# Kernel optimization log

Hardware: AMD Instinct MI355X
Metric: run time of the kernel (lower is better)

The kernel has to match this reference:

```python
import jax, jax.numpy as jnp
import numpy as np

EPS = 1e-7  # K.epsilon()


def setup_inputs() -> dict:
    key = jax.random.key(0)
    k1, k2, k3, k4 = jax.random.split(key, 4)
    B, T, S = 512, 32, 2048  # batch, time_steps, seq_len
    inputs = jax.random.normal(k1, (B, T, S), dtype=jnp.float32)
    # Keras mask (float 0/1), same shape as inputs
    mask = (jax.random.uniform(k2, (B, T, S)) < 0.8).astype(jnp.float32)
    # 'uniform' keras initializer: U(-0.05, 0.05)
    W = jax.random.uniform(k3, (S, T, T), minval=-0.05, maxval=0.05, dtype=jnp.float32)
    b = jax.random.uniform(k4, (S, T), minval=-0.05, maxval=0.05, dtype=jnp.float32)
    return {"inputs": inputs, "mask": mask, "W": W, "b": b}


def reference(inputs, mask, W, b):
    # (B,T,S) -> (B,S,T), apply mask
    x = jnp.transpose(inputs, (0, 2, 1)) * jnp.transpose(mask, (0, 2, 1))
    # per-position matmul, batched over B and S (replaces the tf.scan over batch)
    z = jnp.einsum('bst,stu->bsu', x, W) + b  # (B,S,T)
    e = jnp.exp(jnp.tanh(z))
    att = e / (jnp.sum(e, axis=2, keepdims=True) + EPS)  # softmax-like over T
    return jnp.sum(att * x, axis=1)  # (B,T)
```

## Files before the change

### kernel.cpp

```cpp
#include <hip/hip_runtime.h>

#define EPS_K 1e-7f

typedef __attribute__((ext_vector_type(8)))  short          frag8;
typedef __attribute__((ext_vector_type(16))) float          accf16;
typedef __attribute__((ext_vector_type(4)))  unsigned short us4;

__device__ __forceinline__ unsigned f2bf(float f) {
  union { float f; unsigned u; } v; v.f = f;
  unsigned u = v.u;
  u += 0x7FFFu + ((u >> 16) & 1u);
  return u >> 16;
}
__device__ __forceinline__ float bf2f(unsigned short s) {
  union { unsigned u; float f; } v; v.u = ((unsigned)s) << 16;
  return v.f;
}
__device__ __forceinline__ unsigned pk_bf16(float lo, float hi) {
  return f2bf(lo) | (f2bf(hi) << 16);
}

__global__ __launch_bounds__(256) void wbf_prep(
    const float* __restrict__ Wt, unsigned short* __restrict__ Wbf)
{
  __shared__ unsigned short tile[32 * 33];
  const int s   = blockIdx.x;
  const int tid = threadIdx.x;
  {
    const int t  = tid >> 3;
    const int uc = tid & 7;
    const float4 v = *(const float4*)(Wt + s * 1024 + t * 32 + 4 * uc);
    tile[t * 33 + 4 * uc + 0] = (unsigned short)f2bf(v.x);
    tile[t * 33 + 4 * uc + 1] = (unsigned short)f2bf(v.y);
    tile[t * 33 + 4 * uc + 2] = (unsigned short)f2bf(v.z);
    tile[t * 33 + 4 * uc + 3] = (unsigned short)f2bf(v.w);
  }
  __syncthreads();
  {
    const int u  = tid >> 3;
    const int tc = tid & 7;
    uint2 d;
    d.x = (unsigned)tile[(4 * tc + 0) * 33 + u] | ((unsigned)tile[(4 * tc + 1) * 33 + u] << 16);
    d.y = (unsigned)tile[(4 * tc + 2) * 33 + u] | ((unsigned)tile[(4 * tc + 3) * 33 + u] << 16);
    *(uint2*)(Wbf + s * 1024 + u * 32 + 4 * tc) = d;
  }
}

template <bool WBF, bool USE_WS>
__global__ __launch_bounds__(256, 5) void attn_fused(
    const float* __restrict__ inp,
    const float* __restrict__ msk,
    const float* __restrict__ Wt,
    const unsigned short* __restrict__ Wbf,
    const float* __restrict__ bias,
    float* __restrict__ part,
    float* __restrict__ out)
{
  __shared__ unsigned short x_us[32 * 512];

  const int tid = threadIdx.x;
  const int st  = blockIdx.x >> 4;
  const int bg  = blockIdx.x & 15;
  const int s0  = st * 16;

  #pragma unroll
  for (int iter = 0; iter < 2; ++iter) {
    const int idx = iter * 256 + tid;
    const int sc  = idx & 3;
    const int tb  = (idx >> 2) & 3;
    const int b   = idx >> 4;
    const float* ip = inp + ((size_t)(bg * 32 + b) * 32 + 8 * tb) * 2048 + s0 + 4 * sc;
    const float* mp = msk + ((size_t)(bg * 32 + b) * 32 + 8 * tb) * 2048 + s0 + 4 * sc;
    unsigned c32[4][4];
    #pragma unroll
    for (int j2 = 0; j2 < 4; ++j2) {
      const float4 vi0 = *(const float4*)(ip + (2 * j2)     * 2048);
      const float4 vm0 = *(const float4*)(mp + (2 * j2)     * 2048);
      const float4 vi1 = *(const float4*)(ip + (2 * j2 + 1) * 2048);
      const float4 vm1 = *(const float4*)(mp + (2 * j2 + 1) * 2048);
      c32[0][j2] = pk_bf16(vi0.x * vm0.x, vi1.x * vm1.x);
      c32[1][j2] = pk_bf16(vi0.y * vm0.y, vi1.y * vm1.y);
      c32[2][j2] = pk_bf16(vi0.z * vm0.z, vi1.z * vm1.z);
      c32[3][j2] = pk_bf16(vi0.w * vm0.w, vi1.w * vm1.w);
    }
    #pragma unroll
    for (int w = 0; w < 4; ++w) {
      const int L = tb * 16 + 4 * sc + w;
      unsigned* dst = (unsigned*)(x_us + b * 512 + ((L ^ (b & 7)) * 8));
      *(uint4*)dst = make_uint4(c32[w][0], c32[w][1], c32[w][2], c32[w][3]);
    }
  }
  __syncthreads();

  const int lane = tid & 63;
  const int wv   = tid >> 6;
  const int n    = lane & 31;
  const int h    = lane >> 5;
  const int nx   = n & 7;

  float O[16];
  #pragma unroll
  for (int r = 0; r < 16; ++r) O[r] = 0.f;

  #pragma unroll
  for (int si = 0; si < 4; ++si) {
    const int sl = wv * 4 + si;
    const int s  = s0 + sl;

    frag8 a1, a2;
    if (WBF) {
      const unsigned short* wp = Wbf + s * 1024 + n * 32 + 8 * h;
      a1 = *(const frag8*)(wp);
      a2 = *(const frag8*)(wp + 16);
    } else {
      const float* Wp = Wt + s * 1024;
      #pragma unroll
      for (int j = 0; j < 8; ++j) {
        const int t1 = 8 * h + j;
        a1[j] = (short)f2bf(Wp[t1 * 32 + n]);
        a2[j] = (short)f2bf(Wp[(t1 + 16) * 32 + n]);
      }
    }

    const frag8 b1 = *(const frag8*)(x_us + n * 512 + (((h      * 16 + sl) ^ nx) * 8));
    const frag8 b2 = *(const frag8*)(x_us + n * 512 + ((((h + 2) * 16 + sl) ^ nx) * 8));

    accf16 acc;
    #pragma unroll
    for (int g = 0; g < 4; ++g) {
      const float4 bb = *(const float4*)(bias + s * 32 + 8 * g + 4 * h);
      acc[4 * g + 0] = bb.x; acc[4 * g + 1] = bb.y;
      acc[4 * g + 2] = bb.z; acc[4 * g + 3] = bb.w;
    }
    acc = __builtin_amdgcn_mfma_f32_32x32x16_bf16(a1, b1, acc, 0, 0, 0);
    acc = __builtin_amdgcn_mfma_f32_32x32x16_bf16(a2, b2, acc, 0, 0, 0);

    float e[16];
    float ps = 0.f;
    #pragma unroll
    for (int r = 0; r < 16; ++r) {
      const float z  = acc[r];
      const float e2 = __expf(2.f * z);
      const float th = 1.f - 2.f / (e2 + 1.f);
      e[r] = __expf(th);
      ps  += e[r];
    }
    const float tot = ps + __shfl_xor(ps, 32, 64);
    const float inv = 1.f / (tot + EPS_K);

    #pragma unroll
    for (int g = 0; g < 4; ++g) {
      const us4 xv = *(const us4*)(x_us + n * 512 + (((g * 16 + sl) ^ nx) * 8) + 4 * h);
      #pragma unroll
      for (int i = 0; i < 4; ++i)
        O[4 * g + i] += e[4 * g + i] * inv * bf2f(xv[i]);
    }
  }

  __syncthreads();
  float* red = (float*)x_us;
  #pragma unroll
  for (int r = 0; r < 16; ++r) {
    const int u = (r & 3) + 8 * (r >> 2) + 4 * h;
    red[wv * 1024 + n * 32 + (u ^ n)] = O[r];
  }
  __syncthreads();

  const int q0 = tid * 4;
  float4 v;
  float* vp = (float*)&v;
  #pragma unroll
  for (int i = 0; i < 4; ++i) {
    const int q = q0 + i;
    const int b = q >> 5, u = q & 31;
    float sum = 0.f;
    #pragma unroll
    for (int w = 0; w < 4; ++w) sum += red[w * 1024 + b * 32 + (u ^ b)];
    vp[i] = sum;
  }
  if (USE_WS) {
    *(float4*)(part + (size_t)st * 16384 + bg * 1024 + q0) = v;
  } else {
    float* op = out + bg * 1024 + q0;
    #pragma unroll
    for (int i = 0; i < 4; ++i) atomicAdd(op + i, vp[i]);
  }
}

__global__ __launch_bounds__(256) void reduce_part(
    const float* __restrict__ part, float* __restrict__ out)
{
  const int f = blockIdx.x * 256 + threadIdx.x;
  float s = 0.f;
  #pragma unroll 8
  for (int st = 0; st < 128; ++st) s += part[(size_t)st * 16384 + f];
  out[f] = s;
}

extern "C" void kernel_launch(void* const* d_in, const int* in_sizes, int n_in,
                              void* d_out, int out_size, void* d_ws, size_t ws_size,
                              hipStream_t stream) {
  const float* inp  = (const float*)d_in[0];
  const float* msk  = (const float*)d_in[1];
  const float* Wt   = (const float*)d_in[2];
  const float* bias = (const float*)d_in[3];
  float* out = (float*)d_out;

  const size_t part_sz = (size_t)128 * 16384 * sizeof(float);
  const size_t wbf_sz  = (size_t)2048 * 1024 * sizeof(unsigned short);

  if (ws_size >= part_sz + wbf_sz) {
    float* part = (float*)d_ws;
    unsigned short* Wbf = (unsigned short*)((char*)d_ws + part_sz);
    wbf_prep<<<dim3(2048), dim3(256), 0, stream>>>(Wt, Wbf);
    attn_fused<true, true><<<dim3(2048), dim3(256), 0, stream>>>(
        inp, msk, Wt, Wbf, bias, part, out);
    reduce_part<<<dim3(64), dim3(256), 0, stream>>>(part, out);
  } else if (ws_size >= part_sz) {
    float* part = (float*)d_ws;
    attn_fused<false, true><<<dim3(2048), dim3(256), 0, stream>>>(
        inp, msk, Wt, nullptr, bias, part, out);
    reduce_part<<<dim3(64), dim3(256), 0, stream>>>(part, out);
  } else {
    (void)hipMemsetAsync(out, 0, (size_t)out_size * sizeof(float), stream);
    attn_fused<false, false><<<dim3(2048), dim3(256), 0, stream>>>(
        inp, msk, Wt, nullptr, bias, nullptr, out);
  }
}
```

Baseline: 332.2 us.

## Halve per-block sequence tile, double grid, reduce via atomics instead of partials

Each block now handles 8 sequence positions instead of 16, so the grid doubles to 4096 blocks and LDS per block halves, which allows more resident blocks. The partial-sum workspace and the separate reduce kernel are removed. Each block instead atomically adds its results into a zeroed output, and the exp results reuse the accumulator registers. This trades one extra launch and the partial-buffer traffic for 4096×1024 float atomics, which can contend and make the summation order nondeterministic.

Result: faster. 322.2 us (-3.0%).

```diff
diff --git a/kernel.cpp b/kernel.cpp
--- a/kernel.cpp
+++ b/kernel.cpp
@@ -46,29 +46,26 @@
   }
 }
 
-template <bool WBF, bool USE_WS>
+template <bool WBF>
 __global__ __launch_bounds__(256, 5) void attn_fused(
     const float* __restrict__ inp,
     const float* __restrict__ msk,
     const float* __restrict__ Wt,
     const unsigned short* __restrict__ Wbf,
     const float* __restrict__ bias,
-    float* __restrict__ part,
     float* __restrict__ out)
 {
-  __shared__ unsigned short x_us[32 * 512];
+  __shared__ unsigned short x_us[32 * 256];
 
   const int tid = threadIdx.x;
   const int st  = blockIdx.x >> 4;
   const int bg  = blockIdx.x & 15;
-  const int s0  = st * 16;
+  const int s0  = st * 8;
 
-  #pragma unroll
-  for (int iter = 0; iter < 2; ++iter) {
-    const int idx = iter * 256 + tid;
-    const int sc  = idx & 3;
-    const int tb  = (idx >> 2) & 3;
-    const int b   = idx >> 4;
+  {
+    const int sc = tid & 1;
+    const int tb = (tid >> 1) & 3;
+    const int b  = tid >> 3;
     const float* ip = inp + ((size_t)(bg * 32 + b) * 32 + 8 * tb) * 2048 + s0 + 4 * sc;
     const float* mp = msk + ((size_t)(bg * 32 + b) * 32 + 8 * tb) * 2048 + s0 + 4 * sc;
     unsigned c32[4][4];
@@ -85,8 +82,8 @@
     }
     #pragma unroll
     for (int w = 0; w < 4; ++w) {
-      const int L = tb * 16 + 4 * sc + w;
-      unsigned* dst = (unsigned*)(x_us + b * 512 + ((L ^ (b & 7)) * 8));
+      const int L = tb * 8 + 4 * sc + w;
+      unsigned* dst = (unsigned*)(x_us + b * 256 + ((L ^ (b & 7)) * 8));
       *(uint4*)dst = make_uint4(c32[w][0], c32[w][1], c32[w][2], c32[w][3]);
     }
   }
@@ -103,8 +100,8 @@
   for (int r = 0; r < 16; ++r) O[r] = 0.f;
 
   #pragma unroll
-  for (int si = 0; si < 4; ++si) {
-    const int sl = wv * 4 + si;
+  for (int si = 0; si < 2; ++si) {
+    const int sl = wv * 2 + si;
     const int s  = s0 + sl;
 
     frag8 a1, a2;
@@ -122,8 +119,8 @@
       }
     }
 
-    const frag8 b1 = *(const frag8*)(x_us + n * 512 + (((h      * 16 + sl) ^ nx) * 8));
-    const frag8 b2 = *(const frag8*)(x_us + n * 512 + ((((h + 2) * 16 + sl) ^ nx) * 8));
+    const frag8 b1 = *(const frag8*)(x_us + n * 256 + (((h      * 8 + sl) ^ nx) * 8));
+    const frag8 b2 = *(const frag8*)(x_us + n * 256 + ((((h + 2) * 8 + sl) ^ nx) * 8));
 
     accf16 acc;
     #pragma unroll
@@ -135,25 +132,24 @@
     acc = __builtin_amdgcn_mfma_f32_32x32x16_bf16(a1, b1, acc, 0, 0, 0);
     acc = __builtin_amdgcn_mfma_f32_32x32x16_bf16(a2, b2, acc, 0, 0, 0);
 
-    float e[16];
     float ps = 0.f;
     #pragma unroll
     for (int r = 0; r < 16; ++r) {
       const float z  = acc[r];
       const float e2 = __expf(2.f * z);
       const float th = 1.f - 2.f / (e2 + 1.f);
-      e[r] = __expf(th);
-      ps  += e[r];
+      acc[r] = __expf(th);
+      ps    += acc[r];
     }
     const float tot = ps + __shfl_xor(ps, 32, 64);
     const float inv = 1.f / (tot + EPS_K);
 
     #pragma unroll
     for (int g = 0; g < 4; ++g) {
-      const us4 xv = *(const us4*)(x_us + n * 512 + (((g * 16 + sl) ^ nx) * 8) + 4 * h);
+      const us4 xv = *(const us4*)(x_us + n * 256 + (((g * 8 + sl) ^ nx) * 8) + 4 * h);
       #pragma unroll
       for (int i = 0; i < 4; ++i)
-        O[4 * g + i] += e[4 * g + i] * inv * bf2f(xv[i]);
+        O[4 * g + i] += acc[4 * g + i] * inv * bf2f(xv[i]);
     }
   }
 
@@ -167,8 +163,6 @@
   __syncthreads();
 
   const int q0 = tid * 4;
-  float4 v;
-  float* vp = (float*)&v;
   #pragma unroll
   for (int i = 0; i < 4; ++i) {
     const int q = q0 + i;
@@ -176,25 +170,8 @@
     float sum = 0.f;
     #pragma unroll
     for (int w = 0; w < 4; ++w) sum += red[w * 1024 + b * 32 + (u ^ b)];
-    vp[i] = sum;
+    atomicAdd(out + bg * 1024 + q, sum);
   }
-  if (USE_WS) {
-    *(float4*)(part + (size_t)st * 16384 + bg * 1024 + q0) = v;
-  } else {
-    float* op = out + bg * 1024 + q0;
-    #pragma unroll
-    for (int i = 0; i < 4; ++i) atomicAdd(op + i, vp[i]);
-  }
-}
-
-__global__ __launch_bounds__(256) void reduce_part(
-    const float* __restrict__ part, float* __restrict__ out)
-{
-  const int f = blockIdx.x * 256 + threadIdx.x;
-  float s = 0.f;
-  #pragma unroll 8
-  for (int st = 0; st < 128; ++st) s += part[(size_t)st * 16384 + f];
-  out[f] = s;
 }
 
 extern "C" void kernel_launch(void* const* d_in, const int* in_sizes, int n_in,
@@ -206,24 +183,17 @@
   const float* bias = (const float*)d_in[3];
   float* out = (float*)d_out;
 
-  const size_t part_sz = (size_t)128 * 16384 * sizeof(float);
-  const size_t wbf_sz  = (size_t)2048 * 1024 * sizeof(unsigned short);
+  const size_t wbf_sz = (size_t)2048 * 1024 * sizeof(unsigned short);
 
-  if (ws_size >= part_sz + wbf_sz) {
-    float* part = (float*)d_ws;
-    unsigned short* Wbf = (unsigned short*)((char*)d_ws + part_sz);
+  (void)hipMemsetAsync(out, 0, (size_t)out_size * sizeof(float), stream);
+
+  if (ws_size >= wbf_sz) {
+    unsigned short* Wbf = (unsigned short*)d_ws;
     wbf_prep<<<dim3(2048), dim3(256), 0, stream>>>(Wt, Wbf);
-    attn_fused<true, true><<<dim3(2048), dim3(256), 0, stream>>>(
-        inp, msk, Wt, Wbf, bias, part, out);
-    reduce_part<<<dim3(64), dim3(256), 0, stream>>>(part, out);
-  } else if (ws_size >= part_sz) {
-    float* part = (float*)d_ws;
-    attn_fused<false, true><<<dim3(2048), dim3(256), 0, stream>>>(
-        inp, msk, Wt, nullptr, bias, part, out);
-    reduce_part<<<dim3(64), dim3(256), 0, stream>>>(part, out);
+    attn_fused<true><<<dim3(4096), dim3(256), 0, stream>>>(
+        inp, msk, Wt, Wbf, bias, out);
   } else {
-    (void)hipMemsetAsync(out, 0, (size_t)out_size * sizeof(float), stream);
-    attn_fused<false, false><<<dim3(2048), dim3(256), 0, stream>>>(
-        inp, msk, Wt, nullptr, bias, nullptr, out);
+    attn_fused<false><<<dim3(4096), dim3(256), 0, stream>>>(
+        inp, msk, Wt, nullptr, bias, out);
   }
 }
```

## Persist blocks over four batch groups with register-prefetched double-buffered x tiles

Applied to the files above, without the earlier changes.

Each block now handles four batch groups for one sequence tile, so the grid drops from 2048 to 512 blocks. W fragments and bias are loaded once per block and reused across the groups, and bias is staged in LDS. Global loads of input and mask are software-pipelined through two register sets into a double-buffered LDS tile, so memory traffic overlaps MFMA and softmax work. Divisions are replaced with hardware reciprocals. The cost is more registers and LDS (occupancy hint lowered to 2), fewer blocks for latency hiding, and extra barriers per group.

Measured after the change: 322.4 us. 3.0% less time.

```diff
diff --git a/kernel.cpp b/kernel.cpp
--- a/kernel.cpp
+++ b/kernel.cpp
@@ -5,6 +5,7 @@
 typedef __attribute__((ext_vector_type(8)))  short          frag8;
 typedef __attribute__((ext_vector_type(16))) float          accf16;
 typedef __attribute__((ext_vector_type(4)))  unsigned short us4;
+typedef __attribute__((ext_vector_type(4)))  float          f32x4;
 
 __device__ __forceinline__ unsigned f2bf(float f) {
   union { float f; unsigned u; } v; v.f = f;
@@ -18,6 +19,9 @@
 }
 __device__ __forceinline__ unsigned pk_bf16(float lo, float hi) {
   return f2bf(lo) | (f2bf(hi) << 16);
+}
+__device__ __forceinline__ float rcp_f(float x) {
+  return __builtin_amdgcn_rcpf(x);
 }
 
 __global__ __launch_bounds__(256) void wbf_prep(
@@ -47,7 +51,7 @@
 }
 
 template <bool WBF, bool USE_WS>
-__global__ __launch_bounds__(256, 5) void attn_fused(
+__global__ __launch_bounds__(256, 2) void attn_fused(
     const float* __restrict__ inp,
     const float* __restrict__ msk,
     const float* __restrict__ Wt,
@@ -56,41 +60,17 @@
     float* __restrict__ part,
     float* __restrict__ out)
 {
-  __shared__ unsigned short x_us[32 * 512];
+  __shared__ unsigned short x_us[2][32 * 512];
+  __shared__ float bias_sm[512];
 
   const int tid = threadIdx.x;
-  const int st  = blockIdx.x >> 4;
-  const int bg  = blockIdx.x & 15;
+  const int st  = blockIdx.x & 127;
+  const int bgq = blockIdx.x >> 7;
   const int s0  = st * 16;
 
-  #pragma unroll
-  for (int iter = 0; iter < 2; ++iter) {
-    const int idx = iter * 256 + tid;
-    const int sc  = idx & 3;
-    const int tb  = (idx >> 2) & 3;
-    const int b   = idx >> 4;
-    const float* ip = inp + ((size_t)(bg * 32 + b) * 32 + 8 * tb) * 2048 + s0 + 4 * sc;
-    const float* mp = msk + ((size_t)(bg * 32 + b) * 32 + 8 * tb) * 2048 + s0 + 4 * sc;
-    unsigned c32[4][4];
-    #pragma unroll
-    for (int j2 = 0; j2 < 4; ++j2) {
-      const float4 vi0 = *(const float4*)(ip + (2 * j2)     * 2048);
-      const float4 vm0 = *(const float4*)(mp + (2 * j2)     * 2048);
-      const float4 vi1 = *(const float4*)(ip + (2 * j2 + 1) * 2048);
-      const float4 vm1 = *(const float4*)(mp + (2 * j2 + 1) * 2048);
-      c32[0][j2] = pk_bf16(vi0.x * vm0.x, vi1.x * vm1.x);
-      c32[1][j2] = pk_bf16(vi0.y * vm0.y, vi1.y * vm1.y);
-      c32[2][j2] = pk_bf16(vi0.z * vm0.z, vi1.z * vm1.z);
-      c32[3][j2] = pk_bf16(vi0.w * vm0.w, vi1.w * vm1.w);
-    }
-    #pragma unroll
-    for (int w = 0; w < 4; ++w) {
-      const int L = tb * 16 + 4 * sc + w;
-      unsigned* dst = (unsigned*)(x_us + b * 512 + ((L ^ (b & 7)) * 8));
-      *(uint4*)dst = make_uint4(c32[w][0], c32[w][1], c32[w][2], c32[w][3]);
-    }
-  }
-  __syncthreads();
+  const int sc = tid & 3;
+  const int tq = (tid >> 2) & 7;
+  const int bq = tid >> 5;
 
   const int lane = tid & 63;
   const int wv   = tid >> 6;
@@ -98,93 +78,153 @@
   const int h    = lane >> 5;
   const int nx   = n & 7;
 
+  *(float2*)(bias_sm + 2 * tid) = *(const float2*)(bias + st * 512 + 2 * tid);
+
+  frag8 a1[4], a2[4];
+  if (WBF) {
+    #pragma unroll
+    for (int p = 0; p < 4; ++p) {
+      const unsigned short* wp = Wbf + (size_t)(s0 + wv * 4 + p) * 1024 + n * 32 + 8 * h;
+      a1[p] = *(const frag8*)(wp);
+      a2[p] = *(const frag8*)(wp + 16);
+    }
+  } else {
+    #pragma unroll
+    for (int p = 0; p < 4; ++p) {
+      const float* Wp = Wt + (size_t)(s0 + wv * 4 + p) * 1024;
+      #pragma unroll
+      for (int j = 0; j < 8; ++j) {
+        a1[p][j] = (short)f2bf(Wp[(8 * h + j) * 32 + n]);
+        a2[p][j] = (short)f2bf(Wp[(8 * h + j + 16) * 32 + n]);
+      }
+    }
+  }
+
+  f32x4 viA0, viA1, viA2, viA3, vmA0, vmA1, vmA2, vmA3;
+  f32x4 viB0, viB1, viB2, viB3, vmB0, vmB1, vmB2, vmB3;
+
+#define LOADX(S, ph) do {                                                     \
+    const int ti_ = (ph) >> 2, ck_ = (ph) & 3;                                \
+    const size_t ro_ = ((size_t)((bgq * 4 + ti_) * 32 + 8 * ck_ + bq) * 32    \
+                       + 4 * tq) * 2048 + s0 + 4 * sc;                        \
+    const float* ip_ = inp + ro_;                                             \
+    const float* mp_ = msk + ro_;                                             \
+    vi##S##0 = *(const f32x4*)(ip_);        vm##S##0 = *(const f32x4*)(mp_);  \
+    vi##S##1 = *(const f32x4*)(ip_ + 2048); vm##S##1 = *(const f32x4*)(mp_ + 2048); \
+    vi##S##2 = *(const f32x4*)(ip_ + 4096); vm##S##2 = *(const f32x4*)(mp_ + 4096); \
+    vi##S##3 = *(const f32x4*)(ip_ + 6144); vm##S##3 = *(const f32x4*)(mp_ + 6144); \
+  } while (0)
+
+#define WRITEX(S, ph) do {                                                    \
+    const int ti_ = (ph) >> 2, ck_ = (ph) & 3;                                \
+    const int b_ = 8 * ck_ + bq;                                              \
+    unsigned short* xb_ = &x_us[ti_ & 1][0] + b_ * 512 + 4 * (tq & 1);        \
+    _Pragma("unroll")                                                         \
+    for (int w = 0; w < 4; ++w) {                                             \
+      const int L_ = (tq >> 1) * 16 + 4 * sc + w;                             \
+      uint2 d_;                                                               \
+      d_.x = pk_bf16(vi##S##0[w] * vm##S##0[w], vi##S##1[w] * vm##S##1[w]);   \
+      d_.y = pk_bf16(vi##S##2[w] * vm##S##2[w], vi##S##3[w] * vm##S##3[w]);   \
+      *(uint2*)(xb_ + (L_ ^ (b_ & 7)) * 8) = d_;                              \
+    }                                                                         \
+  } while (0)
+
+#define SYNC do {                                                             \
+    asm volatile("s_waitcnt lgkmcnt(0)" ::: "memory");                        \
+    __builtin_amdgcn_s_barrier();                                             \
+    asm volatile("" ::: "memory");                                            \
+  } while (0)
+
   float O[16];
   #pragma unroll
   for (int r = 0; r < 16; ++r) O[r] = 0.f;
 
-  #pragma unroll
-  for (int si = 0; si < 4; ++si) {
-    const int sl = wv * 4 + si;
-    const int s  = s0 + sl;
-
-    frag8 a1, a2;
-    if (WBF) {
-      const unsigned short* wp = Wbf + s * 1024 + n * 32 + 8 * h;
-      a1 = *(const frag8*)(wp);
-      a2 = *(const frag8*)(wp + 16);
+  LOADX(A, 0); LOADX(B, 1); WRITEX(A, 0);
+  LOADX(A, 2); WRITEX(B, 1);
+  LOADX(B, 3); WRITEX(A, 2); WRITEX(B, 3);
+  LOADX(B, 4);
+  SYNC;
+
+#define PHASE(P, SL, SW) do {                                                 \
+    const int ph_l = ti * 4 + (P) + 5;                                        \
+    if (ph_l < 16) LOADX(SL, ph_l);                                           \
+    const int ph_w = ti * 4 + (P) + 4;                                        \
+    if (ph_w < 16) WRITEX(SW, ph_w);                                          \
+    const int sl = wv * 4 + (P);                                              \
+    const unsigned short* xb = &x_us[ti & 1][0];                              \
+    const frag8 b1 = *(const frag8*)(xb + n * 512 + (((h    ) * 16 + sl) ^ nx) * 8); \
+    const frag8 b2 = *(const frag8*)(xb + n * 512 + (((h + 2) * 16 + sl) ^ nx) * 8); \
+    accf16 acc;                                                               \
+    _Pragma("unroll")                                                         \
+    for (int g = 0; g < 4; ++g) {                                             \
+      const f32x4 bb = *(const f32x4*)(bias_sm + sl * 32 + 8 * g + 4 * h);    \
+      acc[4 * g + 0] = bb[0]; acc[4 * g + 1] = bb[1];                         \
+      acc[4 * g + 2] = bb[2]; acc[4 * g + 3] = bb[3];                         \
+    }                                                                         \
+    acc = __builtin_amdgcn_mfma_f32_32x32x16_bf16(a1[(P)], b1, acc, 0, 0, 0); \
+    acc = __builtin_amdgcn_mfma_f32_32x32x16_bf16(a2[(P)], b2, acc, 0, 0, 0); \
+    float ps = 0.f;                                                           \
+    _Pragma("unroll")                                                         \
+    for (int r = 0; r < 16; ++r) {                                            \
+      const float z  = acc[r];                                                \
+      const float e2 = __expf(2.f * z);                                       \
+      const float th = 1.f - 2.f * rcp_f(e2 + 1.f);                           \
+      acc[r] = __expf(th);                                                    \
+      ps    += acc[r];                                                        \
+    }                                                                         \
+    const float tot = ps + __shfl_xor(ps, 32, 64);                            \
+    const float inv = rcp_f(tot + EPS_K);                                     \
+    _Pragma("unroll")                                                         \
+    for (int g = 0; g < 4; ++g) {                                             \
+      const us4 xv = *(const us4*)(xb + n * 512 + (((g * 16 + sl) ^ nx) * 8) + 4 * h); \
+      _Pragma("unroll")                                                       \
+      for (int i = 0; i < 4; ++i)                                             \
+        O[4 * g + i] += acc[4 * g + i] * inv * bf2f(xv[i]);                   \
+    }                                                                         \
+  } while (0)
+
+  #pragma unroll 1
+  for (int ti = 0; ti < 4; ++ti) {
+    PHASE(0, A, B);
+    PHASE(1, B, A);
+    PHASE(2, A, B);
+    PHASE(3, B, A);
+
+    SYNC;
+    float* red = (float*)&x_us[ti & 1][0];
+    #pragma unroll
+    for (int r = 0; r < 16; ++r) {
+      const int u = (r & 3) + 8 * (r >> 2) + 4 * h;
+      red[wv * 1024 + n * 32 + (u ^ n)] = O[r];
+      O[r] = 0.f;
+    }
+    SYNC;
+    const int q0 = tid * 4;
+    f32x4 v;
+    #pragma unroll
+    for (int i = 0; i < 4; ++i) {
+      const int q = q0 + i;
+      const int b = q >> 5, u = q & 31;
+      float sum = 0.f;
+      #pragma unroll
+      for (int w = 0; w < 4; ++w) sum += red[w * 1024 + b * 32 + (u ^ b)];
+      v[i] = sum;
+    }
+    const int bg = bgq * 4 + ti;
+    if (USE_WS) {
+      *(f32x4*)(part + (size_t)st * 16384 + bg * 1024 + q0) = v;
     } else {
-      const float* Wp = Wt + s * 1024;
+      float* op = out + bg * 1024 + q0;
       #pragma unroll
-      for (int j = 0; j < 8; ++j) {
-        const int t1 = 8 * h + j;
-        a1[j] = (short)f2bf(Wp[t1 * 32 + n]);
-        a2[j] = (short)f2bf(Wp[(t1 + 16) * 32 + n]);
-      }
-    }
-
-    const frag8 b1 = *(const frag8*)(x_us + n * 512 + (((h      * 16 + sl) ^ nx) * 8));
-    const frag8 b2 = *(const frag8*)(x_us + n * 512 + ((((h + 2) * 16 + sl) ^ nx) * 8));
-
-    accf16 acc;
-    #pragma unroll
-    for (int g = 0; g < 4; ++g) {
-      const float4 bb = *(const float4*)(bias + s * 32 + 8 * g + 4 * h);
-      acc[4 * g + 0] = bb.x; acc[4 * g + 1] = bb.y;
-      acc[4 * g + 2] = bb.z; acc[4 * g + 3] = bb.w;
-    }
-    acc = __builtin_amdgcn_mfma_f32_32x32x16_bf16(a1, b1, acc, 0, 0, 0);
-    acc = __builtin_amdgcn_mfma_f32_32x32x16_bf16(a2, b2, acc, 0, 0, 0);
-
-    float e[16];
-    float ps = 0.f;
-    #pragma unroll
-    for (int r = 0; r < 16; ++r) {
-      const float z  = acc[r];
-      const float e2 = __expf(2.f * z);
-      const float th = 1.f - 2.f / (e2 + 1.f);
-      e[r] = __expf(th);
-      ps  += e[r];
-    }
-    const float tot = ps + __shfl_xor(ps, 32, 64);
-    const float inv = 1.f / (tot + EPS_K);
-
-    #pragma unroll
-    for (int g = 0; g < 4; ++g) {
-      const us4 xv = *(const us4*)(x_us + n * 512 + (((g * 16 + sl) ^ nx) * 8) + 4 * h);
-      #pragma unroll
-      for (int i = 0; i < 4; ++i)
-        O[4 * g + i] += e[4 * g + i] * inv * bf2f(xv[i]);
-    }
-  }
-
-  __syncthreads();
-  float* red = (float*)x_us;
-  #pragma unroll
-  for (int r = 0; r < 16; ++r) {
-    const int u = (r & 3) + 8 * (r >> 2) + 4 * h;
-    red[wv * 1024 + n * 32 + (u ^ n)] = O[r];
-  }
-  __syncthreads();
-
-  const int q0 = tid * 4;
-  float4 v;
-  float* vp = (float*)&v;
-  #pragma unroll
-  for (int i = 0; i < 4; ++i) {
-    const int q = q0 + i;
-    const int b = q >> 5, u = q & 31;
-    float sum = 0.f;
-    #pragma unroll
-    for (int w = 0; w < 4; ++w) sum += red[w * 1024 + b * 32 + (u ^ b)];
-    vp[i] = sum;
-  }
-  if (USE_WS) {
-    *(float4*)(part + (size_t)st * 16384 + bg * 1024 + q0) = v;
-  } else {
-    float* op = out + bg * 1024 + q0;
-    #pragma unroll
-    for (int i = 0; i < 4; ++i) atomicAdd(op + i, vp[i]);
-  }
+      for (int i = 0; i < 4; ++i) atomicAdd(op + i, v[i]);
+    }
+    SYNC;
+  }
+
+#undef PHASE
+#undef LOADX
+#undef WRITEX
+#undef SYNC
 }
 
 __global__ __launch_bounds__(256) void reduce_part(
@@ -213,17 +253,17 @@
     float* part = (float*)d_ws;
     unsigned short* Wbf = (unsigned short*)((char*)d_ws + part_sz);
     wbf_prep<<<dim3(2048), dim3(256), 0, stream>>>(Wt, Wbf);
-    attn_fused<true, true><<<dim3(2048), dim3(256), 0, stream>>>(
+    attn_fused<true, true><<<dim3(512), dim3(256), 0, stream>>>(
         inp, msk, Wt, Wbf, bias, part, out);
     reduce_part<<<dim3(64), dim3(256), 0, stream>>>(part, out);
   } else if (ws_size >= part_sz) {
     float* part = (float*)d_ws;
-    attn_fused<false, true><<<dim3(2048), dim3(256), 0, stream>>>(
+    attn_fused<false, true><<<dim3(512), dim3(256), 0, stream>>>(
         inp, msk, Wt, nullptr, bias, part, out);
     reduce_part<<<dim3(64), dim3(256), 0, stream>>>(part, out);
   } else {
     (void)hipMemsetAsync(out, 0, (size_t)out_size * sizeof(float), stream);
-    attn_fused<false, false><<<dim3(2048), dim3(256), 0, stream>>>(
+    attn_fused<false, false><<<dim3(512), dim3(256), 0, stream>>>(
         inp, msk, Wt, nullptr, bias, nullptr, out);
   }
 }
```
